# Kernel tuning notes

Measured on AMD Instinct MI355X. Metric: run time of the kernel, lower is better.

The kernel has to match this reference:

```python
import jax, jax.numpy as jnp
import numpy as np

TWO_PI = 2.0 * np.pi
ROTATION_PROB = 0.5


def _rodrigues(axis, angle):
    """Vectorized Rodrigues formula. axis: [G,3] (unnormalized), angle: [G] in [0,1) (scaled by 2pi).
    Returns R: [G,3,3]."""
    ax = axis / jnp.linalg.norm(axis, axis=-1, keepdims=True)
    a0, a1, a2 = ax[:, 0], ax[:, 1], ax[:, 2]
    z = jnp.zeros_like(a0)
    # Skew-symmetric cross-product matrix K per graph: [G,3,3]
    K = jnp.stack([
        jnp.stack([z, -a2, a1], axis=-1),
        jnp.stack([a2, z, -a0], axis=-1),
        jnp.stack([-a1, a0, z], axis=-1),
    ], axis=-2)
    theta = (angle * TWO_PI)[:, None, None]
    I = jnp.eye(3, dtype=axis.dtype)
    return I + jnp.sin(theta) * K + (1.0 - jnp.cos(theta)) * jnp.matmul(K, K)


def setup_inputs() -> dict:
    key = jax.random.key(0)
    ks = jax.random.split(key, 8)
    G, N, E = 8192, 2_000_000, 16_000_000
    x = jax.random.normal(ks[0], (N, 3), dtype=jnp.float32)
    edge_attr = jax.random.normal(ks[1], (E, 3), dtype=jnp.float32)
    y = jax.random.normal(ks[2], (G, 3), dtype=jnp.float32)
    node_batch = jnp.sort(jax.random.randint(ks[3], (N,), 0, G, dtype=jnp.int32))
    edge_batch = jnp.sort(jax.random.randint(ks[4], (E,), 0, G, dtype=jnp.int32))
    axis = jax.random.normal(ks[5], (G, 3), dtype=jnp.float32)
    angle = jax.random.uniform(ks[6], (G,), dtype=jnp.float32)
    apply_rand = jax.random.uniform(ks[7], (G,), dtype=jnp.float32)
    return {"x": x, "edge_attr": edge_attr, "y": y, "node_batch": node_batch,
            "edge_batch": edge_batch, "axis": axis, "angle": angle,
            "apply_rand": apply_rand}


def reference(x, edge_attr, y, node_batch, edge_batch, axis, angle, apply_rand):
    R = _rodrigues(axis, angle)  # [G,3,3]
    I = jnp.eye(3, dtype=x.dtype)
    # Only rotate graphs where the coin flip succeeds (identity otherwise)
    R = jnp.where((apply_rand < ROTATION_PROB)[:, None, None], R, I)
    # v @ R.T  ==  out[n,j] = sum_i v[n,i] * R[j,i]
    x_out = jnp.einsum('ni,nji->nj', x, R[node_batch])
    e_out = jnp.einsum('ei,eji->ej', edge_attr, R[edge_batch])
    y_out = jnp.einsum('gi,gji->gj', y, R)
    return x_out, e_out, y_out
```

## Files before the change

kernel.cpp:

```cpp
#include <hip/hip_runtime.h>
#include <math.h>

#define TWO_PI_F 6.283185307179586f
#define WROWS 256
#define WBLK  64

typedef float f32x4 __attribute__((ext_vector_type(4)));

__global__ void compute_R_kernel(const float* __restrict__ axis,
                                 const float* __restrict__ angle,
                                 const float* __restrict__ apply_rand,
                                 float* __restrict__ R, int G) {
    int g = blockIdx.x * blockDim.x + threadIdx.x;
    if (g >= G) return;
    float a = axis[3 * g + 0];
    float b = axis[3 * g + 1];
    float c = axis[3 * g + 2];
    float inv = rsqrtf(a * a + b * b + c * c);
    a *= inv; b *= inv; c *= inv;
    float th = angle[g] * TWO_PI_F;
    float s, co;
    sincosf(th, &s, &co);
    float omc = 1.0f - co;

    float r00 = 1.0f - omc * (b * b + c * c);
    float r01 = -s * c + omc * (a * b);
    float r02 =  s * b + omc * (a * c);
    float r10 =  s * c + omc * (a * b);
    float r11 = 1.0f - omc * (a * a + c * c);
    float r12 = -s * a + omc * (b * c);
    float r20 = -s * b + omc * (a * c);
    float r21 =  s * a + omc * (b * c);
    float r22 = 1.0f - omc * (a * a + b * b);

    if (!(apply_rand[g] < 0.5f)) {
        r00 = 1.0f; r01 = 0.0f; r02 = 0.0f;
        r10 = 0.0f; r11 = 1.0f; r12 = 0.0f;
        r20 = 0.0f; r21 = 0.0f; r22 = 1.0f;
    }
    float4* Rg = reinterpret_cast<float4*>(R + 12 * (size_t)g);
    Rg[0] = make_float4(r00, r01, r02, 0.0f);
    Rg[1] = make_float4(r10, r11, r12, 0.0f);
    Rg[2] = make_float4(r20, r21, r22, 0.0f);
}

template <bool HAS_BATCH>
__global__ __launch_bounds__(WBLK) void apply_rot_wave(
        const float* __restrict__ v,
        const int* __restrict__ batch,
        const float* __restrict__ R,
        float* __restrict__ out, int n) {
    __shared__ float buf[WROWS * 3];
    float4* buf4 = reinterpret_cast<float4*>(buf);

    const int lane = threadIdx.x;
    const size_t rowBase = (size_t)blockIdx.x * WROWS;
    int rows = n - (int)rowBase;
    if (rows > WROWS) rows = WROWS;
    const int floatsHere = rows * 3;
    const int f4Here = floatsHere >> 2;
    const int tailFloats = floatsHere & 3;
    const int nRow4 = rows >> 2;

    float4 a0 = make_float4(0, 0, 0, 0), a1 = a0, a2 = a0;
    float aT = 0.f;
    {
        const float4* src = reinterpret_cast<const float4*>(v + rowBase * 3);
        if (lane < f4Here)       a0 = src[lane];
        if (lane + 64 < f4Here)  a1 = src[lane + 64];
        if (lane + 128 < f4Here) a2 = src[lane + 128];
        if (tailFloats && lane < tailFloats)
            aT = v[rowBase * 3 + (((size_t)f4Here) << 2) + lane];
    }
    int4 bi = make_int4(0, 0, 0, 0);
    if (lane < nRow4) {
        if (HAS_BATCH) {
            bi = *(reinterpret_cast<const int4*>(batch + rowBase) + lane);
        } else {
            int b = (int)rowBase + 4 * lane;
            bi = make_int4(b, b + 1, b + 2, b + 3);
        }
    }

    if (lane < f4Here)       buf4[lane]       = a0;
    if (lane + 64 < f4Here)  buf4[lane + 64]  = a1;
    if (lane + 128 < f4Here) buf4[lane + 128] = a2;
    if (tailFloats && lane < tailFloats) buf[(f4Here << 2) + lane] = aT;
    __syncthreads();

    if (lane < nRow4) {
        float4 p0 = buf4[3 * lane + 0];
        float4 p1 = buf4[3 * lane + 1];
        float4 p2 = buf4[3 * lane + 2];
        float rowsv[4][3] = {
            {p0.x, p0.y, p0.z},
            {p0.w, p1.x, p1.y},
            {p1.z, p1.w, p2.x},
            {p2.y, p2.z, p2.w}};
        int gs[4] = {bi.x, bi.y, bi.z, bi.w};
        float oo[12];
#pragma unroll
        for (int r = 0; r < 4; ++r) {
            const float4* Rg = reinterpret_cast<const float4*>(R + 12 * (size_t)gs[r]);
            float4 R0 = Rg[0];
            float4 R1 = Rg[1];
            float4 R2 = Rg[2];
            float v0 = rowsv[r][0], v1 = rowsv[r][1], v2 = rowsv[r][2];
            oo[3 * r + 0] = R0.x * v0 + R0.y * v1 + R0.z * v2;
            oo[3 * r + 1] = R1.x * v0 + R1.y * v1 + R1.z * v2;
            oo[3 * r + 2] = R2.x * v0 + R2.y * v1 + R2.z * v2;
        }
        buf4[3 * lane + 0] = make_float4(oo[0], oo[1], oo[2], oo[3]);
        buf4[3 * lane + 1] = make_float4(oo[4], oo[5], oo[6], oo[7]);
        buf4[3 * lane + 2] = make_float4(oo[8], oo[9], oo[10], oo[11]);
    } else if (lane == nRow4 && (rows & 3)) {
        for (int r = nRow4 * 4; r < rows; ++r) {
            size_t row = rowBase + r;
            int g = HAS_BATCH ? batch[row] : (int)row;
            const float* Rg = R + 12 * (size_t)g;
            float v0 = buf[3 * r + 0], v1 = buf[3 * r + 1], v2 = buf[3 * r + 2];
            float t0 = Rg[0] * v0 + Rg[1] * v1 + Rg[2]  * v2;
            float t1 = Rg[4] * v0 + Rg[5] * v1 + Rg[6]  * v2;
            float t2 = Rg[8] * v0 + Rg[9] * v1 + Rg[10] * v2;
            buf[3 * r + 0] = t0; buf[3 * r + 1] = t1; buf[3 * r + 2] = t2;
        }
    }
    __syncthreads();

    {
        const f32x4* b4 = reinterpret_cast<const f32x4*>(buf);
        f32x4* dst = reinterpret_cast<f32x4*>(out + rowBase * 3);
        if (lane < f4Here) {
            f32x4 val = b4[lane];
            __builtin_nontemporal_store(val, &dst[lane]);
        }
        if (lane + 64 < f4Here) {
            f32x4 val = b4[lane + 64];
            __builtin_nontemporal_store(val, &dst[lane + 64]);
        }
        if (lane + 128 < f4Here) {
            f32x4 val = b4[lane + 128];
            __builtin_nontemporal_store(val, &dst[lane + 128]);
        }
        if (tailFloats && lane < tailFloats) {
            int fi = (f4Here << 2) + lane;
            __builtin_nontemporal_store(buf[fi], &out[rowBase * 3 + fi]);
        }
    }
}

extern "C" void kernel_launch(void* const* d_in, const int* in_sizes, int n_in,
                              void* d_out, int out_size, void* d_ws, size_t ws_size,
                              hipStream_t stream) {
    const float* x          = (const float*)d_in[0];
    const float* edge_attr  = (const float*)d_in[1];
    const float* y          = (const float*)d_in[2];
    const int*   node_batch = (const int*)d_in[3];
    const int*   edge_batch = (const int*)d_in[4];
    const float* axis       = (const float*)d_in[5];
    const float* angle      = (const float*)d_in[6];
    const float* apply_rand = (const float*)d_in[7];

    const int N = in_sizes[3];
    const int E = in_sizes[4];
    const int G = in_sizes[6];

    float* R = (float*)d_ws;
    float* x_out = (float*)d_out;
    float* e_out = x_out + 3 * (size_t)N;
    float* y_out = e_out + 3 * (size_t)E;

    compute_R_kernel<<<(G + 255) / 256, 256, 0, stream>>>(
        axis, angle, apply_rand, R, G);

    int nbE = (int)(((size_t)E + WROWS - 1) / WROWS);
    int nbN = (int)(((size_t)N + WROWS - 1) / WROWS);
    int nbG = (int)(((size_t)G + WROWS - 1) / WROWS);

    apply_rot_wave<true><<<nbE, WBLK, 0, stream>>>(edge_attr, edge_batch, R, e_out, E);
    apply_rot_wave<true><<<nbN, WBLK, 0, stream>>>(x, node_batch, R, x_out, N);
    apply_rot_wave<false><<<nbG, WBLK, 0, stream>>>(y, nullptr, R, y_out, G);
}
```

Baseline: 97.27 us.

## Replace per-row batch index reads with segment-start binary search

Adds a small kernel that binary-searches the sorted node and edge batch arrays for the first row of each graph. The rotation kernels then find each block's starting graph by binary search over these starts and walk forward per row, so they no longer stream the full batch index arrays. This removes roughly 4 bytes of DRAM reads per row from a bandwidth-bound kernel. In exchange it adds a serial search per block, an extra launch, and a dependence on the batch arrays being sorted.

```diff
diff --git a/kernel.cpp b/kernel.cpp
--- a/kernel.cpp
+++ b/kernel.cpp
@@ -44,12 +44,30 @@
     Rg[2] = make_float4(r20, r21, r22, 0.0f);
 }
 
+__global__ void bounds_kernel(const int* __restrict__ nb, int N,
+                              const int* __restrict__ eb, int E, int G,
+                              int* __restrict__ nstart,
+                              int* __restrict__ estart) {
+    int i = blockIdx.x * blockDim.x + threadIdx.x;
+    if (i >= 2 * (G + 1)) return;
+    bool isEdge = i > G;
+    int g = isEdge ? i - (G + 1) : i;
+    const int* b = isEdge ? eb : nb;
+    int n = isEdge ? E : N;
+    int lo = 0, hi = n;
+    while (lo < hi) {
+        int mid = (lo + hi) >> 1;
+        if (b[mid] < g) lo = mid + 1; else hi = mid;
+    }
+    if (isEdge) estart[g] = lo; else nstart[g] = lo;
+}
+
 template <bool HAS_BATCH>
 __global__ __launch_bounds__(WBLK) void apply_rot_wave(
         const float* __restrict__ v,
-        const int* __restrict__ batch,
+        const int* __restrict__ start,
         const float* __restrict__ R,
-        float* __restrict__ out, int n) {
+        float* __restrict__ out, int n, int G) {
     __shared__ float buf[WROWS * 3];
     float4* buf4 = reinterpret_cast<float4*>(buf);
 
@@ -72,14 +90,30 @@
         if (tailFloats && lane < tailFloats)
             aT = v[rowBase * 3 + (((size_t)f4Here) << 2) + lane];
     }
-    int4 bi = make_int4(0, 0, 0, 0);
-    if (lane < nRow4) {
-        if (HAS_BATCH) {
-            bi = *(reinterpret_cast<const int4*>(batch + rowBase) + lane);
-        } else {
-            int b = (int)rowBase + 4 * lane;
-            bi = make_int4(b, b + 1, b + 2, b + 3);
-        }
+
+    int gs[4];
+    int gTail = 0;
+    if (HAS_BATCH) {
+        int rb = (int)rowBase;
+        int lo = 0, hi = G;
+        while (lo < hi) {
+            int mid = (lo + hi + 1) >> 1;
+            if (start[mid] <= rb) lo = mid; else hi = mid - 1;
+        }
+        int g = lo;
+        gTail = g;
+        if (lane < nRow4) {
+            int row0 = rb + 4 * lane;
+#pragma unroll
+            for (int r = 0; r < 4; ++r) {
+                int row = row0 + r;
+                while (start[g + 1] <= row) ++g;
+                gs[r] = g;
+            }
+        }
+    } else {
+        int b = (int)rowBase + 4 * lane;
+        gs[0] = b; gs[1] = b + 1; gs[2] = b + 2; gs[3] = b + 3;
     }
 
     if (lane < f4Here)       buf4[lane]       = a0;
@@ -97,7 +131,6 @@
             {p0.w, p1.x, p1.y},
             {p1.z, p1.w, p2.x},
             {p2.y, p2.z, p2.w}};
-        int gs[4] = {bi.x, bi.y, bi.z, bi.w};
         float oo[12];
 #pragma unroll
         for (int r = 0; r < 4; ++r) {
@@ -114,9 +147,11 @@
         buf4[3 * lane + 1] = make_float4(oo[4], oo[5], oo[6], oo[7]);
         buf4[3 * lane + 2] = make_float4(oo[8], oo[9], oo[10], oo[11]);
     } else if (lane == nRow4 && (rows & 3)) {
+        int g = gTail;
         for (int r = nRow4 * 4; r < rows; ++r) {
-            size_t row = rowBase + r;
-            int g = HAS_BATCH ? batch[row] : (int)row;
+            int row = (int)rowBase + r;
+            if (HAS_BATCH) { while (start[g + 1] <= row) ++g; }
+            else g = row;
             const float* Rg = R + 12 * (size_t)g;
             float v0 = buf[3 * r + 0], v1 = buf[3 * r + 1], v2 = buf[3 * r + 2];
             float t0 = Rg[0] * v0 + Rg[1] * v1 + Rg[2]  * v2;
@@ -166,18 +201,22 @@
     const int G = in_sizes[6];
 
     float* R = (float*)d_ws;
+    int* nstart = (int*)(R + 12 * (size_t)G);
+    int* estart = nstart + (G + 1);
     float* x_out = (float*)d_out;
     float* e_out = x_out + 3 * (size_t)N;
     float* y_out = e_out + 3 * (size_t)E;
 
     compute_R_kernel<<<(G + 255) / 256, 256, 0, stream>>>(
         axis, angle, apply_rand, R, G);
+    bounds_kernel<<<(2 * (G + 1) + 255) / 256, 256, 0, stream>>>(
+        node_batch, N, edge_batch, E, G, nstart, estart);
 
     int nbE = (int)(((size_t)E + WROWS - 1) / WROWS);
     int nbN = (int)(((size_t)N + WROWS - 1) / WROWS);
     int nbG = (int)(((size_t)G + WROWS - 1) / WROWS);
 
-    apply_rot_wave<true><<<nbE, WBLK, 0, stream>>>(edge_attr, edge_batch, R, e_out, E);
-    apply_rot_wave<true><<<nbN, WBLK, 0, stream>>>(x, node_batch, R, x_out, N);
-    apply_rot_wave<false><<<nbG, WBLK, 0, stream>>>(y, nullptr, R, y_out, G);
-}
+    apply_rot_wave<true><<<nbE, WBLK, 0, stream>>>(edge_attr, estart, R, e_out, E, G);
+    apply_rot_wave<true><<<nbN, WBLK, 0, stream>>>(x, nstart, R, x_out, N, G);
+    apply_rot_wave<false><<<nbG, WBLK, 0, stream>>>(y, nullptr, R, y_out, G, G);
+}
```

After: 94.19 us. -3.2%, faster.
